# Performance work log

Hardware: AMD Instinct MI355X
Metric: run time of the kernel (lower is better)

Reference implementation:

```python
import jax, jax.numpy as jnp
import numpy as np

N_OBJECTS = 30
N_POINTS = 500
BATCH = 16384
ROT_WEIGHT = 1.0
TRANS_WEIGHT = 1.0


def quat_to_mat(q):
    # q: [B,4] (w,x,y,z) -> [B,3,3]; matches the module's (unnormalized) formula
    w, x, y, z = q[:, 0], q[:, 1], q[:, 2], q[:, 3]
    x2, y2, z2 = x * x, y * y, z * z
    xy, xz, yz = x * y, x * z, y * z
    wx, wy, wz = w * x, w * y, w * z
    row0 = jnp.stack([1 - 2 * y2 - 2 * z2, 2 * xy - 2 * wz, 2 * xz + 2 * wy], axis=1)
    row1 = jnp.stack([2 * xy + 2 * wz, 1 - 2 * x2 - 2 * z2, 2 * yz - 2 * wx], axis=1)
    row2 = jnp.stack([2 * xz - 2 * wy, 2 * yz + 2 * wx, 1 - 2 * x2 - 2 * y2], axis=1)
    return jnp.stack([row0, row1, row2], axis=1)


def setup_inputs() -> dict:
    key = jax.random.key(0)
    k1, k2, k3, k4, k5, k6 = jax.random.split(key, 6)
    pred_r = jax.random.normal(k1, (BATCH, 4), dtype=jnp.float32)
    pred_t = jax.random.normal(k2, (BATCH, 3), dtype=jnp.float32)
    gt_r = jax.random.normal(k3, (BATCH, 4), dtype=jnp.float32)
    gt_t = jax.random.normal(k4, (BATCH, 3), dtype=jnp.float32)
    obj_ids = jax.random.randint(k5, (BATCH,), 0, N_OBJECTS, dtype=jnp.int64)
    # sampled 3D model points per object (stand-in for loaded .ply meshes, in meters)
    points = jax.random.normal(k6, (N_OBJECTS, N_POINTS, 3), dtype=jnp.float32) * 0.1
    return {"pred_r": pred_r, "pred_t": pred_t, "gt_r": gt_r, "gt_t": gt_t,
            "obj_ids": obj_ids, "points": points}


def reference(pred_r, pred_t, gt_r, gt_t, obj_ids, points):
    Rp = quat_to_mat(pred_r)  # [B,3,3]
    Rg = quat_to_mat(gt_r)
    pts = points[obj_ids]  # [B,N,3] gather per-sample model points
    # pts @ R^T for both rotations; the difference is all that's needed for ADD/rot
    rot_diff = jnp.einsum('bij,bnj->bni', Rp - Rg, pts)  # [B,N,3]
    t_diff = pred_t - gt_t  # [B,3]
    add = jnp.linalg.norm(rot_diff + t_diff[:, None, :], axis=-1).mean(axis=1)  # [B]
    rot = jnp.linalg.norm(rot_diff, axis=-1).mean(axis=1)  # [B]
    trans = jnp.linalg.norm(t_diff, axis=-1)  # [B]
    return add.mean() + ROT_WEIGHT * rot.mean() + TRANS_WEIGHT * trans.mean()
```

## Files before the change

### kernel.cpp

```cpp
#include <hip/hip_runtime.h>

#define BATCH 16384
#define NPTS  500
#define NOBJ  30
#define EPW   2
#define WPB   4
#define NBLK  (BATCH / (EPW * WPB))
#define NCTR1 32
#define GRP   (NBLK / NCTR1)
#define CTR_STRIDE 32

typedef float v2f __attribute__((ext_vector_type(2)));

__device__ __forceinline__ float fsqrt(float x) {
    return __builtin_amdgcn_sqrtf(x);
}

#define CTR_INIT 0xAAAAAAAAu

__global__ __launch_bounds__(256) void add_loss_fused(
    const float* __restrict__ pred_r,
    const float* __restrict__ pred_t,
    const float* __restrict__ gt_r,
    const float* __restrict__ gt_t,
    const int*   __restrict__ obj_ids,
    const float* __restrict__ points,
    float*        __restrict__ partial,
    unsigned int* __restrict__ ctr1,
    unsigned int* __restrict__ ctr2,
    float*        __restrict__ out)
{
    const int wave  = threadIdx.x >> 6;
    const int lane  = threadIdx.x & 63;
    const int gwave = blockIdx.x * WPB + wave;
    const int b0    = gwave * EPW;

    float acc_pts   = 0.0f;
    float acc_trans = 0.0f;

    #pragma unroll
    for (int e = 0; e < EPW; ++e) {
        const int b = b0 + e;

        const float4 qp = ((const float4*)pred_r)[b];
        const float4 qg = ((const float4*)gt_r)[b];

        v2f W = {qp.x, qg.x}, X = {qp.y, qg.y}, Y = {qp.z, qg.z}, Z = {qp.w, qg.w};

        v2f t00 = Y*Y + Z*Z;
        v2f t01 = X*Y - W*Z;
        v2f t02 = X*Z + W*Y;
        v2f t10 = X*Y + W*Z;
        v2f t11 = X*X + Z*Z;
        v2f t12 = Y*Z - W*X;
        v2f t20 = X*Z - W*Y;
        v2f t21 = Y*Z + W*X;
        v2f t22 = X*X + Y*Y;

        float d00 = 2.f*(t00.y - t00.x);
        float d01 = 2.f*(t01.x - t01.y);
        float d02 = 2.f*(t02.x - t02.y);
        float d10 = 2.f*(t10.x - t10.y);
        float d11 = 2.f*(t11.y - t11.x);
        float d12 = 2.f*(t12.x - t12.y);
        float d20 = 2.f*(t20.x - t20.y);
        float d21 = 2.f*(t21.x - t21.y);
        float d22 = 2.f*(t22.y - t22.x);

        float tdx = pred_t[3*b+0] - gt_t[3*b+0];
        float tdy = pred_t[3*b+1] - gt_t[3*b+1];
        float tdz = pred_t[3*b+2] - gt_t[3*b+2];

        const int obj = obj_ids[b];
        const float4* __restrict__ P4 = (const float4*)(points + (size_t)obj * (NPTS*3));

        float s = 0.0f;
        #pragma unroll
        for (int t = 0; t < 2; ++t) {
            const int g = t*64 + lane;
            if (t == 0 || lane < 61) {
                float4 a  = P4[3*g+0];
                float4 b4 = P4[3*g+1];
                float4 c  = P4[3*g+2];
                v2f xs[2] = { {a.x, a.w},  {b4.z, c.y} };
                v2f ys[2] = { {a.y, b4.x}, {b4.w, c.z} };
                v2f zs[2] = { {a.z, b4.y}, {c.x, c.w} };
                #pragma unroll
                for (int j = 0; j < 2; ++j) {
                    v2f x = xs[j], y = ys[j], z = zs[j];
                    v2f vx = d00*x + d01*y + d02*z;
                    v2f vy = d10*x + d11*y + d12*z;
                    v2f vz = d20*x + d21*y + d22*z;
                    v2f r  = vx*vx + vy*vy + vz*vz;
                    s += fsqrt(r.x) + fsqrt(r.y);
                    v2f ax = vx + tdx, ay = vy + tdy, az = vz + tdz;
                    v2f r2 = ax*ax + ay*ay + az*az;
                    s += fsqrt(r2.x) + fsqrt(r2.y);
                }
            }
        }

        acc_pts   += s;
        acc_trans += fsqrt(tdx*tdx + tdy*tdy + tdz*tdz);
    }

    #pragma unroll
    for (int off = 32; off > 0; off >>= 1)
        acc_pts += __shfl_down(acc_pts, off, 64);

    __shared__ float red[WPB];
    __shared__ int   is_last;
    if (lane == 0)
        red[wave] = acc_pts * (1.0f / NPTS) + acc_trans;
    __syncthreads();

    if (threadIdx.x == 0) {
        float bsum = red[0] + red[1] + red[2] + red[3];
        __hip_atomic_store(&partial[blockIdx.x], bsum,
                           __ATOMIC_RELAXED, __HIP_MEMORY_SCOPE_AGENT);
        asm volatile("s_waitcnt vmcnt(0)" ::: "memory");

        unsigned int* c1 = &ctr1[(blockIdx.x & (NCTR1 - 1)) * CTR_STRIDE];
        unsigned int old = __hip_atomic_fetch_add(c1, 1u,
                              __ATOMIC_RELAXED, __HIP_MEMORY_SCOPE_AGENT);
        int lastall = 0;
        if (old == CTR_INIT + (unsigned)(GRP - 1)) {
            unsigned int old2 = __hip_atomic_fetch_add(ctr2, 1u,
                                  __ATOMIC_RELAXED, __HIP_MEMORY_SCOPE_AGENT);
            lastall = (old2 == CTR_INIT + (unsigned)(NCTR1 - 1));
        }
        is_last = lastall;
    }
    __syncthreads();

    if (is_last) {
        float s = 0.0f;
        #pragma unroll
        for (int k = 0; k < NBLK / 256; ++k)
            s += __hip_atomic_load(&partial[k * 256 + threadIdx.x],
                                   __ATOMIC_RELAXED, __HIP_MEMORY_SCOPE_AGENT);

        #pragma unroll
        for (int off = 32; off > 0; off >>= 1)
            s += __shfl_down(s, off, 64);

        __shared__ float red2[4];
        if (lane == 0) red2[wave] = s;
        __syncthreads();
        if (threadIdx.x == 0)
            out[0] = (red2[0] + red2[1] + red2[2] + red2[3]) * (1.0f / BATCH);
    }
}

extern "C" void kernel_launch(void* const* d_in, const int* in_sizes, int n_in,
                              void* d_out, int out_size, void* d_ws, size_t ws_size,
                              hipStream_t stream) {
    const float* pred_r  = (const float*)d_in[0];
    const float* pred_t  = (const float*)d_in[1];
    const float* gt_r    = (const float*)d_in[2];
    const float* gt_t    = (const float*)d_in[3];
    const int*   obj_ids = (const int*)d_in[4];
    const float* points  = (const float*)d_in[5];
    float*        out     = (float*)d_out;
    float*        partial = (float*)d_ws;
    unsigned int* ctr1    = (unsigned int*)((char*)d_ws + NBLK * sizeof(float));
    unsigned int* ctr2    = (unsigned int*)((char*)d_ws + NBLK * sizeof(float)
                                            + NCTR1 * CTR_STRIDE * sizeof(unsigned int));

    add_loss_fused<<<NBLK, 256, 0, stream>>>(
        pred_r, pred_t, gt_r, gt_t, obj_ids, points, partial, ctr1, ctr2, out);
}
```

Baseline: 71.37 us.

## Hoist all per-element loads ahead of math and make the final reduction hierarchical

All point, translation and quaternion loads for a batch element are issued up front, and the tail block's loads are made unconditional by clamping the index and masking the sum, so more memory requests are in flight before the math starts. Counter groups are now contiguous ranges of 64 blocks. The last block of each group reduces its 64 partials and writes a group sum, and the last group leader reduces the 32 group sums, so no single block serially loads all 2048 partials. Launch bounds now request 8 blocks per CU, which may limit registers. The extra preloaded float4s raise register pressure.

```diff
diff --git a/kernel.cpp b/kernel.cpp
--- a/kernel.cpp
+++ b/kernel.cpp
@@ -6,8 +6,8 @@
 #define EPW   2
 #define WPB   4
 #define NBLK  (BATCH / (EPW * WPB))
-#define NCTR1 32
-#define GRP   (NBLK / NCTR1)
+#define NGRP  32
+#define GRP   (NBLK / NGRP)
 #define CTR_STRIDE 32
 
 typedef float v2f __attribute__((ext_vector_type(2)));
@@ -18,7 +18,7 @@
 
 #define CTR_INIT 0xAAAAAAAAu
 
-__global__ __launch_bounds__(256) void add_loss_fused(
+__global__ __launch_bounds__(256, 8) void add_loss_fused(
     const float* __restrict__ pred_r,
     const float* __restrict__ pred_t,
     const float* __restrict__ gt_r,
@@ -28,12 +28,15 @@
     float*        __restrict__ partial,
     unsigned int* __restrict__ ctr1,
     unsigned int* __restrict__ ctr2,
+    float*        __restrict__ gsum,
     float*        __restrict__ out)
 {
-    const int wave  = threadIdx.x >> 6;
-    const int lane  = threadIdx.x & 63;
-    const int gwave = blockIdx.x * WPB + wave;
-    const int b0    = gwave * EPW;
+    const int wave = threadIdx.x >> 6;
+    const int lane = threadIdx.x & 63;
+    const int b0   = (blockIdx.x * WPB + wave) * EPW;
+
+    const float mask1 = (lane < 61) ? 1.0f : 0.0f;
+    const int   g1    = min(64 + lane, 124);
 
     float acc_pts   = 0.0f;
     float acc_trans = 0.0f;
@@ -44,9 +47,14 @@
 
         const float4 qp = ((const float4*)pred_r)[b];
         const float4 qg = ((const float4*)gt_r)[b];
+        const float  tpx = pred_t[3*b+0], tpy = pred_t[3*b+1], tpz = pred_t[3*b+2];
+        const float  tgx = gt_t[3*b+0],   tgy = gt_t[3*b+1],   tgz = gt_t[3*b+2];
+        const int    obj = obj_ids[b];
+        const float4* __restrict__ P4 = (const float4*)(points + (size_t)obj * (NPTS*3));
+        const float4 A0 = P4[3*lane+0], B0 = P4[3*lane+1], C0 = P4[3*lane+2];
+        const float4 A1 = P4[3*g1+0],   B1 = P4[3*g1+1],   C1 = P4[3*g1+2];
 
         v2f W = {qp.x, qg.x}, X = {qp.y, qg.y}, Y = {qp.z, qg.z}, Z = {qp.w, qg.w};
-
         v2f t00 = Y*Y + Z*Z;
         v2f t01 = X*Y - W*Z;
         v2f t02 = X*Z + W*Y;
@@ -56,7 +64,6 @@
         v2f t20 = X*Z - W*Y;
         v2f t21 = Y*Z + W*X;
         v2f t22 = X*X + Y*Y;
-
         float d00 = 2.f*(t00.y - t00.x);
         float d01 = 2.f*(t01.x - t01.y);
         float d02 = 2.f*(t02.x - t02.y);
@@ -66,38 +73,44 @@
         float d20 = 2.f*(t20.x - t20.y);
         float d21 = 2.f*(t21.x - t21.y);
         float d22 = 2.f*(t22.y - t22.x);
-
-        float tdx = pred_t[3*b+0] - gt_t[3*b+0];
-        float tdy = pred_t[3*b+1] - gt_t[3*b+1];
-        float tdz = pred_t[3*b+2] - gt_t[3*b+2];
-
-        const int obj = obj_ids[b];
-        const float4* __restrict__ P4 = (const float4*)(points + (size_t)obj * (NPTS*3));
+        float tdx = tpx - tgx, tdy = tpy - tgy, tdz = tpz - tgz;
 
         float s = 0.0f;
-        #pragma unroll
-        for (int t = 0; t < 2; ++t) {
-            const int g = t*64 + lane;
-            if (t == 0 || lane < 61) {
-                float4 a  = P4[3*g+0];
-                float4 b4 = P4[3*g+1];
-                float4 c  = P4[3*g+2];
-                v2f xs[2] = { {a.x, a.w},  {b4.z, c.y} };
-                v2f ys[2] = { {a.y, b4.x}, {b4.w, c.z} };
-                v2f zs[2] = { {a.z, b4.y}, {c.x, c.w} };
-                #pragma unroll
-                for (int j = 0; j < 2; ++j) {
-                    v2f x = xs[j], y = ys[j], z = zs[j];
-                    v2f vx = d00*x + d01*y + d02*z;
-                    v2f vy = d10*x + d11*y + d12*z;
-                    v2f vz = d20*x + d21*y + d22*z;
-                    v2f r  = vx*vx + vy*vy + vz*vz;
-                    s += fsqrt(r.x) + fsqrt(r.y);
-                    v2f ax = vx + tdx, ay = vy + tdy, az = vz + tdz;
-                    v2f r2 = ax*ax + ay*ay + az*az;
-                    s += fsqrt(r2.x) + fsqrt(r2.y);
-                }
+        {
+            v2f xs[2] = { {A0.x, A0.w}, {B0.z, C0.y} };
+            v2f ys[2] = { {A0.y, B0.x}, {B0.w, C0.z} };
+            v2f zs[2] = { {A0.z, B0.y}, {C0.x, C0.w} };
+            #pragma unroll
+            for (int j = 0; j < 2; ++j) {
+                v2f x = xs[j], y = ys[j], z = zs[j];
+                v2f vx = d00*x + d01*y + d02*z;
+                v2f vy = d10*x + d11*y + d12*z;
+                v2f vz = d20*x + d21*y + d22*z;
+                v2f r  = vx*vx + vy*vy + vz*vz;
+                s += fsqrt(r.x) + fsqrt(r.y);
+                v2f ax = vx + tdx, ay = vy + tdy, az = vz + tdz;
+                v2f r2 = ax*ax + ay*ay + az*az;
+                s += fsqrt(r2.x) + fsqrt(r2.y);
             }
+        }
+        {
+            float s1 = 0.0f;
+            v2f xs[2] = { {A1.x, A1.w}, {B1.z, C1.y} };
+            v2f ys[2] = { {A1.y, B1.x}, {B1.w, C1.z} };
+            v2f zs[2] = { {A1.z, B1.y}, {C1.x, C1.w} };
+            #pragma unroll
+            for (int j = 0; j < 2; ++j) {
+                v2f x = xs[j], y = ys[j], z = zs[j];
+                v2f vx = d00*x + d01*y + d02*z;
+                v2f vy = d10*x + d11*y + d12*z;
+                v2f vz = d20*x + d21*y + d22*z;
+                v2f r  = vx*vx + vy*vy + vz*vz;
+                s1 += fsqrt(r.x) + fsqrt(r.y);
+                v2f ax = vx + tdx, ay = vy + tdy, az = vz + tdz;
+                v2f r2 = ax*ax + ay*ay + az*az;
+                s1 += fsqrt(r2.x) + fsqrt(r2.y);
+            }
+            s += mask1 * s1;
         }
 
         acc_pts   += s;
@@ -109,46 +122,54 @@
         acc_pts += __shfl_down(acc_pts, off, 64);
 
     __shared__ float red[WPB];
-    __shared__ int   is_last;
+    __shared__ int   flag;
     if (lane == 0)
         red[wave] = acc_pts * (1.0f / NPTS) + acc_trans;
+    if (threadIdx.x == 0) flag = 0;
     __syncthreads();
+
+    const int grp = blockIdx.x >> 6;
 
     if (threadIdx.x == 0) {
         float bsum = red[0] + red[1] + red[2] + red[3];
         __hip_atomic_store(&partial[blockIdx.x], bsum,
                            __ATOMIC_RELAXED, __HIP_MEMORY_SCOPE_AGENT);
         asm volatile("s_waitcnt vmcnt(0)" ::: "memory");
-
-        unsigned int* c1 = &ctr1[(blockIdx.x & (NCTR1 - 1)) * CTR_STRIDE];
-        unsigned int old = __hip_atomic_fetch_add(c1, 1u,
+        unsigned int old = __hip_atomic_fetch_add(&ctr1[grp * CTR_STRIDE], 1u,
                               __ATOMIC_RELAXED, __HIP_MEMORY_SCOPE_AGENT);
-        int lastall = 0;
-        if (old == CTR_INIT + (unsigned)(GRP - 1)) {
-            unsigned int old2 = __hip_atomic_fetch_add(ctr2, 1u,
-                                  __ATOMIC_RELAXED, __HIP_MEMORY_SCOPE_AGENT);
-            lastall = (old2 == CTR_INIT + (unsigned)(NCTR1 - 1));
-        }
-        is_last = lastall;
+        if (old == CTR_INIT + (unsigned)(GRP - 1)) flag = 1;
     }
     __syncthreads();
 
-    if (is_last) {
-        float s = 0.0f;
-        #pragma unroll
-        for (int k = 0; k < NBLK / 256; ++k)
-            s += __hip_atomic_load(&partial[k * 256 + threadIdx.x],
-                                   __ATOMIC_RELAXED, __HIP_MEMORY_SCOPE_AGENT);
-
+    if (flag && wave == 0) {
+        float v = __hip_atomic_load(&partial[grp * GRP + lane],
+                                    __ATOMIC_RELAXED, __HIP_MEMORY_SCOPE_AGENT);
         #pragma unroll
         for (int off = 32; off > 0; off >>= 1)
-            s += __shfl_down(s, off, 64);
+            v += __shfl_down(v, off, 64);
 
-        __shared__ float red2[4];
-        if (lane == 0) red2[wave] = s;
-        __syncthreads();
-        if (threadIdx.x == 0)
-            out[0] = (red2[0] + red2[1] + red2[2] + red2[3]) * (1.0f / BATCH);
+        int lastall = 0;
+        if (lane == 0) {
+            __hip_atomic_store(&gsum[grp], v,
+                               __ATOMIC_RELAXED, __HIP_MEMORY_SCOPE_AGENT);
+            asm volatile("s_waitcnt vmcnt(0)" ::: "memory");
+            unsigned int old2 = __hip_atomic_fetch_add(ctr2, 1u,
+                                  __ATOMIC_RELAXED, __HIP_MEMORY_SCOPE_AGENT);
+            lastall = (old2 == CTR_INIT + (unsigned)(NGRP - 1)) ? 1 : 0;
+        }
+        lastall = __shfl(lastall, 0, 64);
+
+        if (lastall) {
+            float w = 0.0f;
+            if (lane < NGRP)
+                w = __hip_atomic_load(&gsum[lane],
+                                      __ATOMIC_RELAXED, __HIP_MEMORY_SCOPE_AGENT);
+            #pragma unroll
+            for (int off = 32; off > 0; off >>= 1)
+                w += __shfl_down(w, off, 64);
+            if (lane == 0)
+                out[0] = w * (1.0f / BATCH);
+        }
     }
 }
 
@@ -161,12 +182,16 @@
     const float* gt_t    = (const float*)d_in[3];
     const int*   obj_ids = (const int*)d_in[4];
     const float* points  = (const float*)d_in[5];
-    float*        out     = (float*)d_out;
-    float*        partial = (float*)d_ws;
-    unsigned int* ctr1    = (unsigned int*)((char*)d_ws + NBLK * sizeof(float));
-    unsigned int* ctr2    = (unsigned int*)((char*)d_ws + NBLK * sizeof(float)
-                                            + NCTR1 * CTR_STRIDE * sizeof(unsigned int));
+    float* out = (float*)d_out;
+
+    char* ws = (char*)d_ws;
+    float*        partial = (float*)ws;
+    unsigned int* ctr1    = (unsigned int*)(ws + NBLK * sizeof(float));
+    unsigned int* ctr2    = (unsigned int*)(ws + NBLK * sizeof(float)
+                                            + NGRP * CTR_STRIDE * sizeof(unsigned int));
+    float*        gsum    = (float*)(ws + NBLK * sizeof(float)
+                                     + NGRP * CTR_STRIDE * sizeof(unsigned int) + 128);
 
     add_loss_fused<<<NBLK, 256, 0, stream>>>(
-        pred_r, pred_t, gt_r, gt_t, obj_ids, points, partial, ctr1, ctr2, out);
+        pred_r, pred_t, gt_r, gt_t, obj_ids, points, partial, ctr1, ctr2, gsum, out);
 }
```

New measurement: 74.26 us. 1.04x slower.
